# Kernel optimization log

Hardware: AMD Instinct MI355X
Metric: run time of the kernel (lower is better)

## Reference

```python
import jax, jax.numpy as jnp
import numpy as np

HIDDEN = 2048
N_HEADS = 32
N_KV_HEADS = 8
HEAD_DIM = HIDDEN // N_HEADS  # 64
N_REP = N_HEADS // N_KV_HEADS  # 4
ROPE_THETA = 10000.0


def setup_inputs() -> dict:
    key = jax.random.key(0)
    ks = jax.random.split(key, 6)
    B, S = 1, 2048
    scale = 0.02
    return {
        "hidden_states": jax.random.normal(ks[0], (B, S, HIDDEN), dtype=jnp.float32),
        "Wq": jax.random.normal(ks[1], (HIDDEN, N_HEADS * HEAD_DIM), dtype=jnp.float32) * scale,
        "Wk": jax.random.normal(ks[2], (HIDDEN, N_KV_HEADS * HEAD_DIM), dtype=jnp.float32) * scale,
        "Wv": jax.random.normal(ks[3], (HIDDEN, N_KV_HEADS * HEAD_DIM), dtype=jnp.float32) * scale,
        "Wo": jax.random.normal(ks[4], (HIDDEN, HIDDEN), dtype=jnp.float32) * scale,
        "position_ids": jnp.arange(S, dtype=jnp.int64 if jax.config.jax_enable_x64 else jnp.int32)[None, :],
    }


def _rope_cos_sin(position_ids, dtype):
    # inv_freq: [head_dim//2]
    inv_freq = 1.0 / (ROPE_THETA ** (jnp.arange(0, HEAD_DIM, 2, dtype=jnp.float32) / HEAD_DIM))
    # freqs: [B, S, head_dim//2]
    freqs = position_ids.astype(jnp.float32)[:, :, None] * inv_freq[None, None, :]
    emb = jnp.concatenate([freqs, freqs], axis=-1)  # [B, S, head_dim]
    return jnp.cos(emb).astype(dtype), jnp.sin(emb).astype(dtype)


def _rotate_half(x):
    x1, x2 = jnp.split(x, 2, axis=-1)
    return jnp.concatenate([-x2, x1], axis=-1)


def reference(hidden_states, Wq, Wk, Wv, Wo, position_ids):
    B, S, _ = hidden_states.shape
    # projections -> [B, H, S, D]
    q = (hidden_states @ Wq).reshape(B, S, N_HEADS, HEAD_DIM).transpose(0, 2, 1, 3)
    k = (hidden_states @ Wk).reshape(B, S, N_KV_HEADS, HEAD_DIM).transpose(0, 2, 1, 3)
    v = (hidden_states @ Wv).reshape(B, S, N_KV_HEADS, HEAD_DIM).transpose(0, 2, 1, 3)

    cos, sin = _rope_cos_sin(position_ids, hidden_states.dtype)
    cos = cos[:, None, :, :]  # [B,1,S,D]
    sin = sin[:, None, :, :]
    q = q * cos + _rotate_half(q) * sin
    k = k * cos + _rotate_half(k) * sin

    # GQA: expand kv heads
    k = jnp.repeat(k, N_REP, axis=1)  # [B, H, S, D]
    v = jnp.repeat(v, N_REP, axis=1)

    scores = jnp.einsum("bhqd,bhkd->bhqk", q, k) / np.sqrt(HEAD_DIM).astype(np.float32)
    # additive causal mask
    causal = jnp.tril(jnp.ones((S, S), dtype=bool))
    scores = jnp.where(causal[None, None, :, :], scores, jnp.finfo(jnp.float32).min)
    attn = jax.nn.softmax(scores.astype(jnp.float32), axis=-1).astype(q.dtype)

    out = jnp.einsum("bhqk,bhkd->bhqd", attn, v)  # [B,H,S,D]
    out = out.transpose(0, 2, 1, 3).reshape(B, S, HIDDEN)
    return out @ Wo
```

## Files before the change

### kernel.cpp

```cpp
#include <hip/hip_runtime.h>
#include <stdint.h>

typedef __attribute__((ext_vector_type(8))) short short8;
typedef __attribute__((ext_vector_type(4))) float floatx4;
typedef __attribute__((ext_vector_type(16))) float floatx16;

__device__ __forceinline__ float b2f(unsigned short u) {
    union { unsigned int i; float f; } x; x.i = ((unsigned int)u) << 16; return x.f;
}
__device__ __forceinline__ unsigned short f2b(float f) {
    unsigned int x = __float_as_uint(f);
    return (unsigned short)((x + 0x7FFFu + ((x >> 16) & 1u)) >> 16);
}
__device__ __forceinline__ unsigned int cvt_pk_bf16(float lo, float hi) {
    unsigned int r;
    asm("v_cvt_pk_bf16_f32 %0, %1, %2" : "=v"(r) : "v"(lo), "v"(hi));
    return r;
}
__device__ __forceinline__ float exp2_(float x) {
    float r;
    asm("v_exp_f32 %0, %1" : "=v"(r) : "v"(x));
    return r;
}

__device__ __forceinline__ float ldf(const float* p) { return *p; }
__device__ __forceinline__ float ldf(const unsigned short* p) { return b2f(*p); }

__device__ __forceinline__ void gload_lds16(const void* g, void* l) {
    __builtin_amdgcn_global_load_lds((const __attribute__((address_space(1))) unsigned int*)g,
                                     (__attribute__((address_space(3))) unsigned int*)l, 16, 0, 0);
}

__global__ void cast_kernel(const float* __restrict__ in, unsigned short* __restrict__ out, int n) {
    int i = (blockIdx.x * blockDim.x + threadIdx.x) * 4;
    if (i + 3 < n) {
        float4 v = *reinterpret_cast<const float4*>(in + i);
        out[i + 0] = f2b(v.x);
        out[i + 1] = f2b(v.y);
        out[i + 2] = f2b(v.z);
        out[i + 3] = f2b(v.w);
    }
}

template<typename T>
__global__ void transpose_to_bf16(const T* __restrict__ in, unsigned short* __restrict__ out,
                                  int ld_in, int ld_out) {
    __shared__ float tile[64][65];
    int tx = threadIdx.x & 63, ty = threadIdx.x >> 6;
    int c0 = blockIdx.x * 64, r0 = blockIdx.y * 64;
    #pragma unroll
    for (int i = 0; i < 64; i += 4)
        tile[ty + i][tx] = ldf(&in[(size_t)(r0 + ty + i) * ld_in + c0 + tx]);
    __syncthreads();
    #pragma unroll
    for (int i = 0; i < 64; i += 4)
        out[(size_t)(c0 + ty + i) * ld_out + r0 + tx] = f2b(tile[tx][ty + i]);
}

template<int OF32>
__global__ __launch_bounds__(256)
void gemm64x128(const unsigned short* __restrict__ A, const unsigned short* __restrict__ BT,
                void* __restrict__ Cout, int M, int N, int K) {
    __shared__ __align__(16) unsigned short As[2][64 * 64];
    __shared__ __align__(16) unsigned short Bs[2][128 * 64];
    int tid = threadIdx.x;
    int l = tid & 63, w = tid >> 6;
    int lr = l & 15, lg = l >> 4;

    int gx = gridDim.x;
    int nwg = gx * gridDim.y;
    int flat = blockIdx.y * gx + blockIdx.x;
    int q8 = nwg >> 3;
    int f2 = (flat & 7) * q8 + (flat >> 3);
    int bx = f2 % gx, by = f2 / gx;
    int nb = bx * 128, mb = by * 64;

    floatx4 acc[4][2];
    #pragma unroll
    for (int m = 0; m < 4; ++m)
        #pragma unroll
        for (int f = 0; f < 2; ++f) acc[m][f] = (floatx4)(0.f);

    int ca1 = tid + 256;
    int ra0 = tid >> 3, ja0 = (tid & 7) ^ (ra0 & 7);
    int ra1 = ca1 >> 3, ja1 = (ca1 & 7) ^ (ra1 & 7);
    const unsigned short* Ag0 = A + (size_t)(mb + ra0) * K + ja0 * 8;
    const unsigned short* Ag1 = A + (size_t)(mb + ra1) * K + ja1 * 8;
    const unsigned short* Bg[4];
    #pragma unroll
    for (int i = 0; i < 4; ++i) {
        int c = tid + 256 * i;
        int r = c >> 3, j = (c & 7) ^ (r & 7);
        Bg[i] = BT + (size_t)(nb + r) * K + j * 8;
    }

    auto stage = [&](int buf, int kb) {
        gload_lds16(Ag0 + kb, &As[buf][tid * 8]);
        gload_lds16(Ag1 + kb, &As[buf][ca1 * 8]);
        #pragma unroll
        for (int i = 0; i < 4; ++i)
            gload_lds16(Bg[i] + kb, &Bs[buf][(tid + 256 * i) * 8]);
    };

    int nsteps = K >> 6;
    stage(0, 0);
    for (int it = 0; it < nsteps; ++it) {
        int nxt = (it + 1 < nsteps) ? it + 1 : it;
        stage((it + 1) & 1, nxt * 64);
        asm volatile("s_waitcnt vmcnt(6)" ::: "memory");
        __builtin_amdgcn_s_barrier();
        __builtin_amdgcn_sched_barrier(0);

        const unsigned short* Ab = As[it & 1];
        const unsigned short* Bb = Bs[it & 1];
        #pragma unroll
        for (int kh = 0; kh < 2; ++kh) {
            int sl = ((kh * 4 + lg) ^ (lr & 7)) * 8;
            short8 af[4], bf[2];
            #pragma unroll
            for (int m = 0; m < 4; ++m)
                af[m] = *reinterpret_cast<const short8*>(Ab + (m * 16 + lr) * 64 + sl);
            #pragma unroll
            for (int f = 0; f < 2; ++f)
                bf[f] = *reinterpret_cast<const short8*>(Bb + (w * 32 + f * 16 + lr) * 64 + sl);
            #pragma unroll
            for (int m = 0; m < 4; ++m)
                #pragma unroll
                for (int f = 0; f < 2; ++f)
                    acc[m][f] = __builtin_amdgcn_mfma_f32_16x16x32_bf16(af[m], bf[f], acc[m][f], 0, 0, 0);
        }
        __builtin_amdgcn_sched_barrier(0);
        __builtin_amdgcn_s_barrier();
    }
    asm volatile("s_waitcnt vmcnt(0)" ::: "memory");

    #pragma unroll
    for (int m = 0; m < 4; ++m) {
        int orow = mb + m * 16 + lg * 4;
        #pragma unroll
        for (int f = 0; f < 2; ++f) {
            int ocol = nb + w * 32 + f * 16 + lr;
            #pragma unroll
            for (int r = 0; r < 4; ++r) {
                if (OF32)
                    ((float*)Cout)[(size_t)(orow + r) * N + ocol] = acc[m][f][r];
                else
                    ((unsigned short*)Cout)[(size_t)(orow + r) * N + ocol] = f2b(acc[m][f][r]);
            }
        }
    }
}

__global__ void rope_kernel(unsigned short* __restrict__ x, const int* __restrict__ pos_ids,
                            int H, int stride, float scale) {
    int idx = blockIdx.x * blockDim.x + threadIdx.x;
    int i = idx & 31;
    int h = (idx >> 5) % H;
    int s = idx / (32 * H);
    unsigned short* p = x + (size_t)s * stride + h * 64;
    float x1 = b2f(p[i]), x2 = b2f(p[i + 32]);
    float pos = (float)pos_ids[s];
    float inv = exp2f(-0.41524101186092029f * (float)i);
    float a = pos * inv;
    float sn, cs;
    __sincosf(a, &sn, &cs);
    p[i]      = f2b((x1 * cs - x2 * sn) * scale);
    p[i + 32] = f2b((x2 * cs + x1 * sn) * scale);
}

__global__ __launch_bounds__(128, 2)
void attn_kernel(const unsigned short* __restrict__ QKV,
                 const unsigned short* __restrict__ VT,
                 unsigned short* __restrict__ O) {
    const int S = 2048, LDQ = 3072, HID = 2048;
    __shared__ __align__(16) char smem[17664];
    unsigned short* KlBase = (unsigned short*)smem;
    float* Ms = (float*)smem;

    int tid = threadIdx.x;
    int l = tid & 63, w = tid >> 6;
    int lq = l & 31, hl = l >> 5;
    int b = blockIdx.x;
    int h = b & 31;
    int pi = b >> 5;
    int bH = 63 - pi, bL = pi;
    int nH = (bH >> 1) + 1;
    int kvh = h >> 2;
    int qH = bH * 32 + lq;
    int qL = bL * 32 + lq;

    const unsigned short* Kg = QKV + 2048 + kvh * 64;
    const unsigned short* Vr0 = VT + (size_t)(kvh * 64 + lq) * S + hl * 8;
    const unsigned short* Vr1 = VT + (size_t)(kvh * 64 + 32 + lq) * S + hl * 8;

    auto stageK = [&](int buf, int c0w) {
        unsigned short* Kl = KlBase + (buf * 2 + w) * 2048;
        #pragma unroll
        for (int i = 0; i < 4; ++i) {
            int c = l + 64 * i;
            int kr = c >> 3, ks = (c & 7) ^ (kr & 7);
            gload_lds16(Kg + (size_t)(c0w + kr) * LDQ + ks * 8, &Kl[c * 8]);
        }
    };

    auto process = [&](int buf, int c0w, const short8* qf, int qrow, bool diag,
                       float& m, float& lsum, floatx16* acc,
                       short8 v00, short8 v01, short8 v10, short8 v11) {
        const unsigned short* Kb = KlBase + (buf * 2 + w) * 2048;
        floatx16 st = (floatx16)(0.f);
        __builtin_amdgcn_s_setprio(1);
        #pragma unroll
        for (int dc = 0; dc < 4; ++dc) {
            short8 kf = *reinterpret_cast<const short8*>(
                Kb + lq * 64 + (((dc * 2 + hl) ^ (lq & 7)) * 8));
            st = __builtin_amdgcn_mfma_f32_32x32x16_bf16(kf, qf[dc], st, 0, 0, 0);
        }
        __builtin_amdgcn_s_setprio(0);
        if (diag) {
            #pragma unroll
            for (int r = 0; r < 16; ++r) {
                int key = c0w + (r & 3) + 8 * (r >> 2) + 4 * hl;
                if (key > qrow) st[r] = -1e30f;
            }
        }
        float t0 = fmaxf(fmaxf(st[0], st[1]), fmaxf(st[2], st[3]));
        float t1 = fmaxf(fmaxf(st[4], st[5]), fmaxf(st[6], st[7]));
        float t2 = fmaxf(fmaxf(st[8], st[9]), fmaxf(st[10], st[11]));
        float t3 = fmaxf(fmaxf(st[12], st[13]), fmaxf(st[14], st[15]));
        float tm = fmaxf(fmaxf(t0, t1), fmaxf(t2, t3));
        tm = fmaxf(tm, __shfl_xor(tm, 32));
        if (!__all(tm <= m + 11.5f)) {
            float mn = fmaxf(m, tm);
            float al = exp2_(m - mn);
            lsum *= al;
            acc[0] *= al;
            acc[1] *= al;
            m = mn;
        }
        float p[16];
        #pragma unroll
        for (int r = 0; r < 16; ++r) p[r] = exp2_(st[r] - m);
        float s0 = (p[0] + p[1]) + (p[2] + p[3]);
        float s1 = (p[4] + p[5]) + (p[6] + p[7]);
        float s2 = (p[8] + p[9]) + (p[10] + p[11]);
        float s3 = (p[12] + p[13]) + (p[14] + p[15]);
        float rs = (s0 + s1) + (s2 + s3);
        rs += __shfl_xor(rs, 32);
        lsum += rs;
        unsigned int u[4][2];
        #pragma unroll
        for (int B2 = 0; B2 < 4; ++B2) {
            u[B2][0] = cvt_pk_bf16(p[B2 * 4 + 0], p[B2 * 4 + 1]);
            u[B2][1] = cvt_pk_bf16(p[B2 * 4 + 2], p[B2 * 4 + 3]);
        }
        asm volatile("s_waitcnt vmcnt(4)" ::: "memory");
        #pragma unroll
        for (int kc = 0; kc < 2; ++kc) {
            unsigned int o0 = u[2 * kc][0],     o1 = u[2 * kc][1];
            unsigned int e0 = u[2 * kc + 1][0], e1 = u[2 * kc + 1][1];
            unsigned int t0x = (unsigned int)__shfl((int)o0, l ^ 32);
            unsigned int t1x = (unsigned int)__shfl((int)o1, l ^ 32);
            unsigned int s0p = (unsigned int)__shfl((int)e0, l ^ 32);
            unsigned int s1p = (unsigned int)__shfl((int)e1, l ^ 32);
            union { unsigned int uu[4]; short8 s8; } pf;
            pf.uu[0] = hl ? s0p : o0;
            pf.uu[1] = hl ? s1p : o1;
            pf.uu[2] = hl ? e0 : t0x;
            pf.uu[3] = hl ? e1 : t1x;
            __builtin_amdgcn_s_setprio(1);
            acc[0] = __builtin_amdgcn_mfma_f32_32x32x16_bf16(kc ? v01 : v00, pf.s8, acc[0], 0, 0, 0);
            acc[1] = __builtin_amdgcn_mfma_f32_32x32x16_bf16(kc ? v11 : v10, pf.s8, acc[1], 0, 0, 0);
            __builtin_amdgcn_s_setprio(0);
        }
    };

    short8 qfH[4];
    {
        const unsigned short* QrH = QKV + (size_t)qH * LDQ + h * 64;
        #pragma unroll
        for (int c = 0; c < 4; ++c)
            qfH[c] = *reinterpret_cast<const short8*>(QrH + c * 16 + hl * 8);
    }
    floatx16 accH[2];
    accH[0] = (floatx16)(0.f); accH[1] = (floatx16)(0.f);
    float mH = -1e30f, lH = 0.f;

    stageK(0, w * 32);
    for (int j = 0; j < nH; ++j) {
        int c0w = j * 64 + w * 32;
        short8 v00 = *reinterpret_cast<const short8*>(Vr0 + c0w);
        short8 v01 = *reinterpret_cast<const short8*>(Vr0 + c0w + 16);
        short8 v10 = *reinterpret_cast<const short8*>(Vr1 + c0w);
        short8 v11 = *reinterpret_cast<const short8*>(Vr1 + c0w + 16);
        __builtin_amdgcn_sched_barrier(0);
        int jn = j + 1;
        int tn = (jn < nH) ? jn : 0;
        stageK(jn & 1, tn * 64 + w * 32);
        asm volatile("s_waitcnt vmcnt(8)" ::: "memory");
        __builtin_amdgcn_sched_barrier(0);
        process(j & 1, c0w, qfH, qH, j == nH - 1, mH, lH, accH, v00, v01, v10, v11);
    }

    short8 qfL[4];
    {
        const unsigned short* QrL = QKV + (size_t)qL * LDQ + h * 64;
        #pragma unroll
        for (int c = 0; c < 4; ++c)
            qfL[c] = *reinterpret_cast<const short8*>(QrL + c * 16 + hl * 8);
    }
    floatx16 accL[2];
    accL[0] = (floatx16)(0.f); accL[1] = (floatx16)(0.f);
    float mL = -1e30f, lL = 0.f;

    for (int j = nH; j < 33; ++j) {
        int cur = j - nH;
        int c0w = cur * 64 + w * 32;
        short8 v00 = *reinterpret_cast<const short8*>(Vr0 + c0w);
        short8 v01 = *reinterpret_cast<const short8*>(Vr0 + c0w + 16);
        short8 v10 = *reinterpret_cast<const short8*>(Vr1 + c0w);
        short8 v11 = *reinterpret_cast<const short8*>(Vr1 + c0w + 16);
        __builtin_amdgcn_sched_barrier(0);
        int jn = j + 1;
        int tn = (jn < 33) ? jn - nH : cur;
        stageK(jn & 1, tn * 64 + w * 32);
        asm volatile("s_waitcnt vmcnt(8)" ::: "memory");
        __builtin_amdgcn_sched_barrier(0);
        process(j & 1, c0w, qfL, qL, j == 32, mL, lL, accL, v00, v01, v10, v11);
    }
    asm volatile("s_waitcnt vmcnt(0)" ::: "memory");
    __syncthreads();

    if (w == 1) {
        Ms[l * 69 + 0] = mH; Ms[l * 69 + 1] = lH;
        Ms[l * 69 + 2] = mL; Ms[l * 69 + 3] = lL;
        #pragma unroll
        for (int d = 0; d < 2; ++d)
            #pragma unroll
            for (int r = 0; r < 16; ++r) {
                Ms[l * 69 + 4 + d * 16 + r]  = accH[d][r];
                Ms[l * 69 + 36 + d * 16 + r] = accL[d][r];
            }
    }
    __syncthreads();
    if (w == 0) {
        #pragma unroll
        for (int band = 0; band < 2; ++band) {
            float m0 = band ? mL : mH;
            float l0 = band ? lL : lH;
            const floatx16* acc = band ? accL : accH;
            int moff = band ? 2 : 0;
            int aoff = band ? 36 : 4;
            int qrow = band ? qL : qH;
            float m1 = Ms[l * 69 + moff], l1 = Ms[l * 69 + moff + 1];
            float mm = fmaxf(m0, m1);
            float a0 = exp2_(m0 - mm), a1 = exp2_(m1 - mm);
            float inv = 1.0f / (l0 * a0 + l1 * a1);
            a0 *= inv; a1 *= inv;
            unsigned short* Op = O + (size_t)qrow * HID + h * 64 + hl * 4;
            #pragma unroll
            for (int d = 0; d < 2; ++d)
                #pragma unroll
                for (int g4 = 0; g4 < 4; ++g4) {
                    float v0 = acc[d][g4 * 4 + 0] * a0 + Ms[l * 69 + aoff + d * 16 + g4 * 4 + 0] * a1;
                    float v1 = acc[d][g4 * 4 + 1] * a0 + Ms[l * 69 + aoff + d * 16 + g4 * 4 + 1] * a1;
                    float v2 = acc[d][g4 * 4 + 2] * a0 + Ms[l * 69 + aoff + d * 16 + g4 * 4 + 2] * a1;
                    float v3 = acc[d][g4 * 4 + 3] * a0 + Ms[l * 69 + aoff + d * 16 + g4 * 4 + 3] * a1;
                    unsigned long long pk = (unsigned long long)cvt_pk_bf16(v0, v1)
                                          | ((unsigned long long)cvt_pk_bf16(v2, v3) << 32);
                    *reinterpret_cast<unsigned long long*>(Op + d * 32 + g4 * 8) = pk;
                }
        }
    }
}

extern "C" void kernel_launch(void* const* d_in, const int* in_sizes, int n_in,
                              void* d_out, int out_size, void* d_ws, size_t ws_size,
                              hipStream_t stream) {
    const int S = 2048, HID = 2048, KVD = 512, NQKV = 3072;
    const float* hs = (const float*)d_in[0];
    const float* Wq = (const float*)d_in[1];
    const float* Wk = (const float*)d_in[2];
    const float* Wv = (const float*)d_in[3];
    const float* Wo = (const float*)d_in[4];
    const int* pos  = (const int*)d_in[5];

    char* base = (char*)d_ws;
    auto alloc = [&](size_t bytes) {
        char* r = base;
        base += (bytes + 255) & ~(size_t)255;
        return r;
    };
    unsigned short* hs_b     = (unsigned short*)alloc((size_t)S * HID * 2);
    unsigned short* Wqkv     = (unsigned short*)alloc((size_t)NQKV * HID * 2);
    unsigned short* WoT      = (unsigned short*)alloc((size_t)HID * HID * 2);
    unsigned short* qkv      = (unsigned short*)alloc((size_t)S * NQKV * 2);
    unsigned short* vT       = (unsigned short*)alloc((size_t)KVD * S * 2);
    unsigned short* attn_out = (unsigned short*)alloc((size_t)S * HID * 2);

    cast_kernel<<<(S * HID / 4 + 255) / 256, 256, 0, stream>>>(hs, hs_b, S * HID);

    transpose_to_bf16<float><<<dim3(HID / 64, HID / 64), 256, 0, stream>>>(Wq, Wqkv, HID, HID);
    transpose_to_bf16<float><<<dim3(KVD / 64, HID / 64), 256, 0, stream>>>(Wk, Wqkv + (size_t)2048 * HID, KVD, HID);
    transpose_to_bf16<float><<<dim3(KVD / 64, HID / 64), 256, 0, stream>>>(Wv, Wqkv + (size_t)2560 * HID, KVD, HID);
    transpose_to_bf16<float><<<dim3(HID / 64, HID / 64), 256, 0, stream>>>(Wo, WoT, HID, HID);

    gemm64x128<0><<<dim3(NQKV / 128, S / 64), 256, 0, stream>>>(hs_b, Wqkv, qkv, S, NQKV, HID);

    rope_kernel<<<(S * 32 * 32) / 256, 256, 0, stream>>>(qkv, pos, 32, NQKV, 0.18033688011112042f);
    rope_kernel<<<(S * 8 * 32) / 256, 256, 0, stream>>>(qkv + 2048, pos, 8, NQKV, 1.0f);

    transpose_to_bf16<unsigned short><<<dim3(KVD / 64, S / 64), 256, 0, stream>>>(qkv + 2560, vT, NQKV, S);

    attn_kernel<<<1024, 128, 0, stream>>>(qkv, vT, attn_out);

    gemm64x128<1><<<dim3(HID / 128, S / 64), 256, 0, stream>>>(attn_out, WoT, (float*)d_out, S, HID, HID);
}
```

Before: 146.5 us.

## Replace paired causal band scheduling with one query band per block

The attention kernel previously paired a high and a low 32-row query band in each block so every block did the same amount of causal work (33 key tiles). Now each block handles a single band, with heavier bands launched first (band = 63 - b>>5), and the grid doubles to 2048 blocks. This cuts register pressure from two accumulator sets and shrinks the shared-memory merge area. In exchange, per-block work becomes uneven and there is more per-block overhead, relying on the hardware scheduler to balance the descending-cost ordering.

Measured after the change: 147.2 us. No clear change (+0.5%).

```diff
diff --git a/kernel.cpp b/kernel.cpp
--- a/kernel.cpp
+++ b/kernel.cpp
@@ -182,12 +182,18 @@
     int lq = l & 31, hl = l >> 5;
     int b = blockIdx.x;
     int h = b & 31;
-    int pi = b >> 5;
-    int bH = 63 - pi, bL = pi;
-    int nH = (bH >> 1) + 1;
+    int band = 63 - (b >> 5);
+    int nT = (band >> 1) + 1;
     int kvh = h >> 2;
-    int qH = bH * 32 + lq;
-    int qL = bL * 32 + lq;
+    int qrow = band * 32 + lq;
+
+    short8 qf[4];
+    {
+        const unsigned short* Qr = QKV + (size_t)qrow * LDQ + h * 64;
+        #pragma unroll
+        for (int c = 0; c < 4; ++c)
+            qf[c] = *reinterpret_cast<const short8*>(Qr + c * 16 + hl * 8);
+    }
 
     const unsigned short* Kg = QKV + 2048 + kvh * 64;
     const unsigned short* Vr0 = VT + (size_t)(kvh * 64 + lq) * S + hl * 8;
@@ -203,10 +209,25 @@
         }
     };
 
-    auto process = [&](int buf, int c0w, const short8* qf, int qrow, bool diag,
-                       float& m, float& lsum, floatx16* acc,
-                       short8 v00, short8 v01, short8 v10, short8 v11) {
-        const unsigned short* Kb = KlBase + (buf * 2 + w) * 2048;
+    floatx16 acc[2];
+    acc[0] = (floatx16)(0.f); acc[1] = (floatx16)(0.f);
+    float m_run = -1e30f, l_run = 0.f;
+
+    stageK(0, w * 32);
+    for (int j = 0; j < nT; ++j) {
+        int c0w = j * 64 + w * 32;
+        short8 v00 = *reinterpret_cast<const short8*>(Vr0 + c0w);
+        short8 v01 = *reinterpret_cast<const short8*>(Vr0 + c0w + 16);
+        short8 v10 = *reinterpret_cast<const short8*>(Vr1 + c0w);
+        short8 v11 = *reinterpret_cast<const short8*>(Vr1 + c0w + 16);
+        __builtin_amdgcn_sched_barrier(0);
+        int jn = j + 1;
+        int tn = (jn < nT) ? jn : j;
+        stageK(jn & 1, tn * 64 + w * 32);
+        asm volatile("s_waitcnt vmcnt(8)" ::: "memory");
+        __builtin_amdgcn_sched_barrier(0);
+
+        const unsigned short* Kb = KlBase + ((j & 1) * 2 + w) * 2048;
         floatx16 st = (floatx16)(0.f);
         __builtin_amdgcn_s_setprio(1);
         #pragma unroll
@@ -216,7 +237,7 @@
             st = __builtin_amdgcn_mfma_f32_32x32x16_bf16(kf, qf[dc], st, 0, 0, 0);
         }
         __builtin_amdgcn_s_setprio(0);
-        if (diag) {
+        if (j == nT - 1) {
             #pragma unroll
             for (int r = 0; r < 16; ++r) {
                 int key = c0w + (r & 3) + 8 * (r >> 2) + 4 * hl;
@@ -229,24 +250,24 @@
         float t3 = fmaxf(fmaxf(st[12], st[13]), fmaxf(st[14], st[15]));
         float tm = fmaxf(fmaxf(t0, t1), fmaxf(t2, t3));
         tm = fmaxf(tm, __shfl_xor(tm, 32));
-        if (!__all(tm <= m + 11.5f)) {
-            float mn = fmaxf(m, tm);
-            float al = exp2_(m - mn);
-            lsum *= al;
+        if (!__all(tm <= m_run + 11.5f)) {
+            float mn = fmaxf(m_run, tm);
+            float al = exp2_(m_run - mn);
+            l_run *= al;
             acc[0] *= al;
             acc[1] *= al;
-            m = mn;
+            m_run = mn;
         }
         float p[16];
         #pragma unroll
-        for (int r = 0; r < 16; ++r) p[r] = exp2_(st[r] - m);
+        for (int r = 0; r < 16; ++r) p[r] = exp2_(st[r] - m_run);
         float s0 = (p[0] + p[1]) + (p[2] + p[3]);
         float s1 = (p[4] + p[5]) + (p[6] + p[7]);
         float s2 = (p[8] + p[9]) + (p[10] + p[11]);
         float s3 = (p[12] + p[13]) + (p[14] + p[15]);
         float rs = (s0 + s1) + (s2 + s3);
         rs += __shfl_xor(rs, 32);
-        lsum += rs;
+        l_run += rs;
         unsigned int u[4][2];
         #pragma unroll
         for (int B2 = 0; B2 < 4; ++B2) {
@@ -272,104 +293,39 @@
             acc[1] = __builtin_amdgcn_mfma_f32_32x32x16_bf16(kc ? v11 : v10, pf.s8, acc[1], 0, 0, 0);
             __builtin_amdgcn_s_setprio(0);
         }
-    };
-
-    short8 qfH[4];
-    {
-        const unsigned short* QrH = QKV + (size_t)qH * LDQ + h * 64;
-        #pragma unroll
-        for (int c = 0; c < 4; ++c)
-            qfH[c] = *reinterpret_cast<const short8*>(QrH + c * 16 + hl * 8);
-    }
-    floatx16 accH[2];
-    accH[0] = (floatx16)(0.f); accH[1] = (floatx16)(0.f);
-    float mH = -1e30f, lH = 0.f;
-
-    stageK(0, w * 32);
-    for (int j = 0; j < nH; ++j) {
-        int c0w = j * 64 + w * 32;
-        short8 v00 = *reinterpret_cast<const short8*>(Vr0 + c0w);
-        short8 v01 = *reinterpret_cast<const short8*>(Vr0 + c0w + 16);
-        short8 v10 = *reinterpret_cast<const short8*>(Vr1 + c0w);
-        short8 v11 = *reinterpret_cast<const short8*>(Vr1 + c0w + 16);
-        __builtin_amdgcn_sched_barrier(0);
-        int jn = j + 1;
-        int tn = (jn < nH) ? jn : 0;
-        stageK(jn & 1, tn * 64 + w * 32);
-        asm volatile("s_waitcnt vmcnt(8)" ::: "memory");
-        __builtin_amdgcn_sched_barrier(0);
-        process(j & 1, c0w, qfH, qH, j == nH - 1, mH, lH, accH, v00, v01, v10, v11);
-    }
-
-    short8 qfL[4];
-    {
-        const unsigned short* QrL = QKV + (size_t)qL * LDQ + h * 64;
-        #pragma unroll
-        for (int c = 0; c < 4; ++c)
-            qfL[c] = *reinterpret_cast<const short8*>(QrL + c * 16 + hl * 8);
-    }
-    floatx16 accL[2];
-    accL[0] = (floatx16)(0.f); accL[1] = (floatx16)(0.f);
-    float mL = -1e30f, lL = 0.f;
-
-    for (int j = nH; j < 33; ++j) {
-        int cur = j - nH;
-        int c0w = cur * 64 + w * 32;
-        short8 v00 = *reinterpret_cast<const short8*>(Vr0 + c0w);
-        short8 v01 = *reinterpret_cast<const short8*>(Vr0 + c0w + 16);
-        short8 v10 = *reinterpret_cast<const short8*>(Vr1 + c0w);
-        short8 v11 = *reinterpret_cast<const short8*>(Vr1 + c0w + 16);
-        __builtin_amdgcn_sched_barrier(0);
-        int jn = j + 1;
-        int tn = (jn < 33) ? jn - nH : cur;
-        stageK(jn & 1, tn * 64 + w * 32);
-        asm volatile("s_waitcnt vmcnt(8)" ::: "memory");
-        __builtin_amdgcn_sched_barrier(0);
-        process(j & 1, c0w, qfL, qL, j == 32, mL, lL, accL, v00, v01, v10, v11);
     }
     asm volatile("s_waitcnt vmcnt(0)" ::: "memory");
     __syncthreads();
 
     if (w == 1) {
-        Ms[l * 69 + 0] = mH; Ms[l * 69 + 1] = lH;
-        Ms[l * 69 + 2] = mL; Ms[l * 69 + 3] = lL;
+        Ms[l * 36 + 0] = m_run;
+        Ms[l * 36 + 1] = l_run;
         #pragma unroll
         for (int d = 0; d < 2; ++d)
             #pragma unroll
-            for (int r = 0; r < 16; ++r) {
-                Ms[l * 69 + 4 + d * 16 + r]  = accH[d][r];
-                Ms[l * 69 + 36 + d * 16 + r] = accL[d][r];
-            }
+            for (int r = 0; r < 16; ++r)
+                Ms[l * 36 + 2 + d * 16 + r] = acc[d][r];
     }
     __syncthreads();
     if (w == 0) {
-        #pragma unroll
-        for (int band = 0; band < 2; ++band) {
-            float m0 = band ? mL : mH;
-            float l0 = band ? lL : lH;
-            const floatx16* acc = band ? accL : accH;
-            int moff = band ? 2 : 0;
-            int aoff = band ? 36 : 4;
-            int qrow = band ? qL : qH;
-            float m1 = Ms[l * 69 + moff], l1 = Ms[l * 69 + moff + 1];
-            float mm = fmaxf(m0, m1);
-            float a0 = exp2_(m0 - mm), a1 = exp2_(m1 - mm);
-            float inv = 1.0f / (l0 * a0 + l1 * a1);
-            a0 *= inv; a1 *= inv;
-            unsigned short* Op = O + (size_t)qrow * HID + h * 64 + hl * 4;
-            #pragma unroll
-            for (int d = 0; d < 2; ++d)
-                #pragma unroll
-                for (int g4 = 0; g4 < 4; ++g4) {
-                    float v0 = acc[d][g4 * 4 + 0] * a0 + Ms[l * 69 + aoff + d * 16 + g4 * 4 + 0] * a1;
-                    float v1 = acc[d][g4 * 4 + 1] * a0 + Ms[l * 69 + aoff + d * 16 + g4 * 4 + 1] * a1;
-                    float v2 = acc[d][g4 * 4 + 2] * a0 + Ms[l * 69 + aoff + d * 16 + g4 * 4 + 2] * a1;
-                    float v3 = acc[d][g4 * 4 + 3] * a0 + Ms[l * 69 + aoff + d * 16 + g4 * 4 + 3] * a1;
-                    unsigned long long pk = (unsigned long long)cvt_pk_bf16(v0, v1)
-                                          | ((unsigned long long)cvt_pk_bf16(v2, v3) << 32);
-                    *reinterpret_cast<unsigned long long*>(Op + d * 32 + g4 * 8) = pk;
-                }
-        }
+        float m1 = Ms[l * 36 + 0], l1 = Ms[l * 36 + 1];
+        float mm = fmaxf(m_run, m1);
+        float a0 = exp2_(m_run - mm), a1 = exp2_(m1 - mm);
+        float inv = 1.0f / (l_run * a0 + l1 * a1);
+        a0 *= inv; a1 *= inv;
+        unsigned short* Op = O + (size_t)qrow * HID + h * 64 + hl * 4;
+        #pragma unroll
+        for (int d = 0; d < 2; ++d)
+            #pragma unroll
+            for (int g4 = 0; g4 < 4; ++g4) {
+                float v0 = acc[d][g4 * 4 + 0] * a0 + Ms[l * 36 + 2 + d * 16 + g4 * 4 + 0] * a1;
+                float v1 = acc[d][g4 * 4 + 1] * a0 + Ms[l * 36 + 2 + d * 16 + g4 * 4 + 1] * a1;
+                float v2 = acc[d][g4 * 4 + 2] * a0 + Ms[l * 36 + 2 + d * 16 + g4 * 4 + 2] * a1;
+                float v3 = acc[d][g4 * 4 + 3] * a0 + Ms[l * 36 + 2 + d * 16 + g4 * 4 + 3] * a1;
+                unsigned long long pk = (unsigned long long)cvt_pk_bf16(v0, v1)
+                                      | ((unsigned long long)cvt_pk_bf16(v2, v3) << 32);
+                *reinterpret_cast<unsigned long long*>(Op + d * 32 + g4 * 8) = pk;
+            }
     }
 }
 
@@ -411,7 +367,7 @@
 
     transpose_to_bf16<unsigned short><<<dim3(KVD / 64, S / 64), 256, 0, stream>>>(qkv + 2560, vT, NQKV, S);
 
-    attn_kernel<<<1024, 128, 0, stream>>>(qkv, vT, attn_out);
+    attn_kernel<<<2048, 128, 0, stream>>>(qkv, vT, attn_out);
 
     gemm64x128<1><<<dim3(HID / 128, S / 64), 256, 0, stream>>>(attn_out, WoT, (float*)d_out, S, HID, HID);
 }
```

## Split attention KV chunks across four waves per block instead of two

Applied to the files above, without the earlier changes.

The attention kernel now launches 256 threads (4 waves) per block. Each iteration handles a 128-key chunk, with each wave taking 32 keys, so the per-wave loop count is roughly halved. LDS grows to hold double-buffered K tiles for four waves. The final merge combines four partial softmax states through shared memory, one band at a time with extra barriers. The goal is more latency hiding and shorter serial chains per wave, at the cost of a heavier cross-wave reduction and more LDS per block, which may reduce occupancy.

Result: slower. 155.6 us (+6.2%).

```diff
diff --git a/kernel.cpp b/kernel.cpp
--- a/kernel.cpp
+++ b/kernel.cpp
@@ -168,12 +168,12 @@
     p[i + 32] = f2b((x2 * cs + x1 * sn) * scale);
 }
 
-__global__ __launch_bounds__(128, 2)
+__global__ __launch_bounds__(256, 2)
 void attn_kernel(const unsigned short* __restrict__ QKV,
                  const unsigned short* __restrict__ VT,
                  unsigned short* __restrict__ O) {
     const int S = 2048, LDQ = 3072, HID = 2048;
-    __shared__ __align__(16) char smem[17664];
+    __shared__ __align__(16) char smem[32768];
     unsigned short* KlBase = (unsigned short*)smem;
     float* Ms = (float*)smem;
 
@@ -184,7 +184,7 @@
     int h = b & 31;
     int pi = b >> 5;
     int bH = 63 - pi, bL = pi;
-    int nH = (bH >> 1) + 1;
+    int nH = (bH >> 2) + 1;
     int kvh = h >> 2;
     int qH = bH * 32 + lq;
     int qL = bL * 32 + lq;
@@ -194,7 +194,7 @@
     const unsigned short* Vr1 = VT + (size_t)(kvh * 64 + 32 + lq) * S + hl * 8;
 
     auto stageK = [&](int buf, int c0w) {
-        unsigned short* Kl = KlBase + (buf * 2 + w) * 2048;
+        unsigned short* Kl = KlBase + (buf * 4 + w) * 2048;
         #pragma unroll
         for (int i = 0; i < 4; ++i) {
             int c = l + 64 * i;
@@ -206,7 +206,7 @@
     auto process = [&](int buf, int c0w, const short8* qf, int qrow, bool diag,
                        float& m, float& lsum, floatx16* acc,
                        short8 v00, short8 v01, short8 v10, short8 v11) {
-        const unsigned short* Kb = KlBase + (buf * 2 + w) * 2048;
+        const unsigned short* Kb = KlBase + (buf * 4 + w) * 2048;
         floatx16 st = (floatx16)(0.f);
         __builtin_amdgcn_s_setprio(1);
         #pragma unroll
@@ -276,10 +276,10 @@
 
     short8 qfH[4];
     {
-        const unsigned short* QrH = QKV + (size_t)qH * LDQ + h * 64;
+        const unsigned short* Qr = QKV + (size_t)qH * LDQ + h * 64;
         #pragma unroll
         for (int c = 0; c < 4; ++c)
-            qfH[c] = *reinterpret_cast<const short8*>(QrH + c * 16 + hl * 8);
+            qfH[c] = *reinterpret_cast<const short8*>(Qr + c * 16 + hl * 8);
     }
     floatx16 accH[2];
     accH[0] = (floatx16)(0.f); accH[1] = (floatx16)(0.f);
@@ -287,15 +287,15 @@
 
     stageK(0, w * 32);
     for (int j = 0; j < nH; ++j) {
-        int c0w = j * 64 + w * 32;
+        int c0w = j * 128 + w * 32;
         short8 v00 = *reinterpret_cast<const short8*>(Vr0 + c0w);
         short8 v01 = *reinterpret_cast<const short8*>(Vr0 + c0w + 16);
         short8 v10 = *reinterpret_cast<const short8*>(Vr1 + c0w);
         short8 v11 = *reinterpret_cast<const short8*>(Vr1 + c0w + 16);
         __builtin_amdgcn_sched_barrier(0);
         int jn = j + 1;
-        int tn = (jn < nH) ? jn : 0;
-        stageK(jn & 1, tn * 64 + w * 32);
+        int c0n = (jn < nH) ? jn * 128 : 0;
+        stageK(jn & 1, c0n + w * 32);
         asm volatile("s_waitcnt vmcnt(8)" ::: "memory");
         __builtin_amdgcn_sched_barrier(0);
         process(j & 1, c0w, qfH, qH, j == nH - 1, mH, lH, accH, v00, v01, v10, v11);
@@ -303,73 +303,87 @@
 
     short8 qfL[4];
     {
-        const unsigned short* QrL = QKV + (size_t)qL * LDQ + h * 64;
+        const unsigned short* Qr = QKV + (size_t)qL * LDQ + h * 64;
         #pragma unroll
         for (int c = 0; c < 4; ++c)
-            qfL[c] = *reinterpret_cast<const short8*>(QrL + c * 16 + hl * 8);
+            qfL[c] = *reinterpret_cast<const short8*>(Qr + c * 16 + hl * 8);
     }
     floatx16 accL[2];
     accL[0] = (floatx16)(0.f); accL[1] = (floatx16)(0.f);
     float mL = -1e30f, lL = 0.f;
 
-    for (int j = nH; j < 33; ++j) {
+    for (int j = nH; j < 17; ++j) {
         int cur = j - nH;
-        int c0w = cur * 64 + w * 32;
+        int c0w = cur * 128 + w * 32;
         short8 v00 = *reinterpret_cast<const short8*>(Vr0 + c0w);
         short8 v01 = *reinterpret_cast<const short8*>(Vr0 + c0w + 16);
         short8 v10 = *reinterpret_cast<const short8*>(Vr1 + c0w);
         short8 v11 = *reinterpret_cast<const short8*>(Vr1 + c0w + 16);
         __builtin_amdgcn_sched_barrier(0);
         int jn = j + 1;
-        int tn = (jn < 33) ? jn - nH : cur;
-        stageK(jn & 1, tn * 64 + w * 32);
+        int c0n = (jn < 17) ? (jn - nH) * 128 : cur * 128;
+        stageK(jn & 1, c0n + w * 32);
         asm volatile("s_waitcnt vmcnt(8)" ::: "memory");
         __builtin_amdgcn_sched_barrier(0);
-        process(j & 1, c0w, qfL, qL, j == 32, mL, lL, accL, v00, v01, v10, v11);
+        process(j & 1, c0w, qfL, qL, j == 16, mL, lL, accL, v00, v01, v10, v11);
     }
     asm volatile("s_waitcnt vmcnt(0)" ::: "memory");
     __syncthreads();
 
-    if (w == 1) {
-        Ms[l * 69 + 0] = mH; Ms[l * 69 + 1] = lH;
-        Ms[l * 69 + 2] = mL; Ms[l * 69 + 3] = lL;
-        #pragma unroll
-        for (int d = 0; d < 2; ++d)
-            #pragma unroll
-            for (int r = 0; r < 16; ++r) {
-                Ms[l * 69 + 4 + d * 16 + r]  = accH[d][r];
-                Ms[l * 69 + 36 + d * 16 + r] = accL[d][r];
+    #pragma unroll
+    for (int band = 0; band < 2; ++band) {
+        float m0 = band ? mL : mH;
+        float l0 = band ? lL : lH;
+        floatx16* acc = band ? accL : accH;
+        int qrow = band ? qL : qH;
+        if (w != 0) {
+            float* Mw = Ms + ((size_t)(w - 1) * 64 + l) * 34;
+            Mw[0] = m0; Mw[1] = l0;
+            #pragma unroll
+            for (int d = 0; d < 2; ++d)
+                #pragma unroll
+                for (int r = 0; r < 16; ++r)
+                    Mw[2 + d * 16 + r] = acc[d][r];
+        }
+        __syncthreads();
+        if (w == 0) {
+            float mm = m0;
+            #pragma unroll
+            for (int p = 0; p < 3; ++p) mm = fmaxf(mm, Ms[((size_t)p * 64 + l) * 34]);
+            float a0 = exp2_(m0 - mm);
+            float ap[3];
+            float L = l0 * a0;
+            #pragma unroll
+            for (int p = 0; p < 3; ++p) {
+                const float* Mp = Ms + ((size_t)p * 64 + l) * 34;
+                ap[p] = exp2_(Mp[0] - mm);
+                L += Mp[1] * ap[p];
             }
-    }
-    __syncthreads();
-    if (w == 0) {
-        #pragma unroll
-        for (int band = 0; band < 2; ++band) {
-            float m0 = band ? mL : mH;
-            float l0 = band ? lL : lH;
-            const floatx16* acc = band ? accL : accH;
-            int moff = band ? 2 : 0;
-            int aoff = band ? 36 : 4;
-            int qrow = band ? qL : qH;
-            float m1 = Ms[l * 69 + moff], l1 = Ms[l * 69 + moff + 1];
-            float mm = fmaxf(m0, m1);
-            float a0 = exp2_(m0 - mm), a1 = exp2_(m1 - mm);
-            float inv = 1.0f / (l0 * a0 + l1 * a1);
-            a0 *= inv; a1 *= inv;
+            float inv = 1.0f / L;
+            a0 *= inv;
+            #pragma unroll
+            for (int p = 0; p < 3; ++p) ap[p] *= inv;
             unsigned short* Op = O + (size_t)qrow * HID + h * 64 + hl * 4;
             #pragma unroll
             for (int d = 0; d < 2; ++d)
                 #pragma unroll
                 for (int g4 = 0; g4 < 4; ++g4) {
-                    float v0 = acc[d][g4 * 4 + 0] * a0 + Ms[l * 69 + aoff + d * 16 + g4 * 4 + 0] * a1;
-                    float v1 = acc[d][g4 * 4 + 1] * a0 + Ms[l * 69 + aoff + d * 16 + g4 * 4 + 1] * a1;
-                    float v2 = acc[d][g4 * 4 + 2] * a0 + Ms[l * 69 + aoff + d * 16 + g4 * 4 + 2] * a1;
-                    float v3 = acc[d][g4 * 4 + 3] * a0 + Ms[l * 69 + aoff + d * 16 + g4 * 4 + 3] * a1;
-                    unsigned long long pk = (unsigned long long)cvt_pk_bf16(v0, v1)
-                                          | ((unsigned long long)cvt_pk_bf16(v2, v3) << 32);
+                    float vv[4];
+                    #pragma unroll
+                    for (int rr = 0; rr < 4; ++rr) {
+                        int r = g4 * 4 + rr;
+                        float s = acc[d][r] * a0;
+                        #pragma unroll
+                        for (int p = 0; p < 3; ++p)
+                            s += Ms[((size_t)p * 64 + l) * 34 + 2 + d * 16 + r] * ap[p];
+                        vv[rr] = s;
+                    }
+                    unsigned long long pk = (unsigned long long)cvt_pk_bf16(vv[0], vv[1])
+                                          | ((unsigned long long)cvt_pk_bf16(vv[2], vv[3]) << 32);
                     *reinterpret_cast<unsigned long long*>(Op + d * 32 + g4 * 8) = pk;
                 }
         }
+        __syncthreads();
     }
 }
 
@@ -411,7 +425,7 @@
 
     transpose_to_bf16<unsigned short><<<dim3(KVD / 64, S / 64), 256, 0, stream>>>(qkv + 2560, vT, NQKV, S);
 
-    attn_kernel<<<1024, 128, 0, stream>>>(qkv, vT, attn_out);
+    attn_kernel<<<1024, 256, 0, stream>>>(qkv, vT, attn_out);
 
     gemm64x128<1><<<dim3(HID / 128, S / 64), 256, 0, stream>>>(attn_out, WoT, (float*)d_out, S, HID, HID);
 }
```
